# Kernel tuning notes

Measured on AMD Instinct MI355X. Metric: run time of the kernel, lower is better.

## Reference

```python
import jax, jax.numpy as jnp
import numpy as np

N, E, D, ED, H, OUT = 50000, 800000, 128, 32, 16, 128
BN_EPS = 1e-5


def setup_inputs() -> dict:
    key = jax.random.key(0)
    ks = jax.random.split(key, 12)
    s = lambda fan_in: 1.0 / np.sqrt(fan_in)

    x = jax.random.normal(ks[0], (N, D), dtype=jnp.float32)
    edge_idx = jax.random.randint(ks[1], (2, E), 0, N, dtype=jnp.int64)
    edge_feat = jax.random.normal(ks[2], (E, ED), dtype=jnp.float32)

    # edge_mlp: Linear(ED,16) -> GELU -> Linear(16,16); weights stored [in,out]
    eW1 = jax.random.uniform(ks[3], (ED, H), minval=-s(ED), maxval=s(ED), dtype=jnp.float32)
    eb1 = jnp.zeros((H,), jnp.float32)
    eW2 = jax.random.uniform(ks[4], (H, H), minval=-s(H), maxval=s(H), dtype=jnp.float32)
    eb2 = jnp.zeros((H,), jnp.float32)

    # ego_proj: Linear(D, D+16, bias=False)
    ego_W = jax.random.uniform(ks[5], (D, D + H), minval=-s(D), maxval=s(D), dtype=jnp.float32)
    eps = jnp.zeros((1,), jnp.float32)

    # node mlp: Linear(D+16, OUT) -> BN(OUT) -> GELU -> Linear(OUT, OUT)
    W1 = jax.random.uniform(ks[6], (D + H, OUT), minval=-s(D + H), maxval=s(D + H), dtype=jnp.float32)
    b1 = jnp.zeros((OUT,), jnp.float32)
    gamma = jnp.ones((OUT,), jnp.float32)
    beta = jnp.zeros((OUT,), jnp.float32)
    W2 = jax.random.uniform(ks[7], (OUT, OUT), minval=-s(OUT), maxval=s(OUT), dtype=jnp.float32)
    b2 = jnp.zeros((OUT,), jnp.float32)

    return dict(x=x, edge_idx=edge_idx, edge_feat=edge_feat,
                eW1=eW1, eb1=eb1, eW2=eW2, eb2=eb2,
                ego_W=ego_W, eps=eps,
                W1=W1, b1=b1, gamma=gamma, beta=beta, W2=W2, b2=b2)


def reference(x, edge_idx, edge_feat, eW1, eb1, eW2, eb2, ego_W, eps,
              W1, b1, gamma, beta, W2, b2):
    src, dst = edge_idx[0], edge_idx[1]
    # edge MLP (exact GELU, matching torch default)
    e_emb = jax.nn.gelu(edge_feat @ eW1 + eb1, approximate=False) @ eW2 + eb2  # [E,16]
    msg = jnp.concatenate([x[src], e_emb], axis=-1)                            # [E, D+16]
    agg = jax.ops.segment_sum(msg, dst, num_segments=x.shape[0])               # [N, D+16]
    out = (1.0 + eps) * (x @ ego_W) + agg
    # node MLP with BatchNorm1d in training mode (batch stats, biased var)
    h = out @ W1 + b1
    mu = jnp.mean(h, axis=0)
    var = jnp.mean((h - mu) ** 2, axis=0)
    h = (h - mu) * jax.lax.rsqrt(var + BN_EPS) * gamma + beta
    h = jax.nn.gelu(h, approximate=False)
    return h @ W2 + b2
```

## Files before the change

kernel.cpp:

```cpp
#include <hip/hip_runtime.h>
#include <hip/hip_bf16.h>

#define N_NODES 50000
#define E_EDGES 800000
#define D_IN    128
#define ED_IN   32
#define H_HID   16
#define D_CAT   144
#define AGG_LD  144
#define BCAP    48
#define BM      64

typedef __attribute__((ext_vector_type(8))) short bf16x8;
typedef __attribute__((ext_vector_type(4))) float f32x4;

__device__ __forceinline__ float gelu_exact(float v) {
    return 0.5f * v * (1.0f + erff(v * 0.70710678118654752f));
}
__device__ __forceinline__ float4 ld4(const float* p) { return *reinterpret_cast<const float4*>(p); }
__device__ __forceinline__ unsigned short f2bf(float f) {
    unsigned u = __float_as_uint(f);
    return (unsigned short)((u + 0x7FFFu + ((u >> 16) & 1u)) >> 16);
}
__device__ __forceinline__ float bflo(unsigned u) { return __uint_as_float(u << 16); }
__device__ __forceinline__ float bfhi(unsigned u) { return __uint_as_float(u & 0xffff0000u); }
__device__ __forceinline__ unsigned packbf2(float lo, float hi) {
    __hip_bfloat162 h = __float22bfloat162_rn(make_float2(lo, hi));
    return *reinterpret_cast<unsigned*>(&h);
}

__global__ void k_prep(const float* __restrict__ egoW, const float* __restrict__ W1,
                       const float* __restrict__ eps, const float* __restrict__ eW2,
                       const float* __restrict__ eb2, const float* __restrict__ W2,
                       unsigned short* __restrict__ BT, unsigned short* __restrict__ W2T,
                       float* __restrict__ ve, int* __restrict__ cnt,
                       float* __restrict__ stats) {
    const int c = threadIdx.x;
    const int d = blockIdx.x;
    if (d < 128) {
        float acc = 0.f;
        for (int j = 0; j < D_CAT; ++j)
            acc = fmaf(egoW[d * D_CAT + j], W1[j * 128 + c], acc);
        BT[c * 288 + d] = f2bf((1.0f + eps[0]) * acc);
    } else if (d == 128) {
        for (int j = 0; j < 128; ++j)
            BT[c * 288 + 128 + j] = f2bf(W1[j * 128 + c]);
        #pragma unroll
        for (int j = 0; j < H_HID; ++j) {
            float s = 0.f;
            #pragma unroll
            for (int k = 0; k < H_HID; ++k)
                s = fmaf(eW2[j * H_HID + k], W1[(D_IN + k) * 128 + c], s);
            BT[c * 288 + 256 + j] = f2bf(s);
        }
        #pragma unroll
        for (int j = 272; j < 288; ++j) BT[c * 288 + j] = 0;
        float s = 0.f;
        #pragma unroll
        for (int k = 0; k < H_HID; ++k)
            s = fmaf(eb2[k], W1[(D_IN + k) * 128 + c], s);
        ve[c] = s;
    } else if (d == 129) {
        for (int k = 0; k < 128; ++k)
            W2T[c * 128 + k] = f2bf(W2[k * 128 + c]);
    } else if (d < 521) {
        int idx = (d - 130) * 128 + c;
        if (idx < N_NODES) cnt[idx] = 0;
    } else {
        stats[c] = 0.f; stats[128 + c] = 0.f;
    }
}

__global__ __launch_bounds__(256) void k_edge(const float* __restrict__ x,
        uint4* __restrict__ xb, const int* __restrict__ eidx,
        const float* __restrict__ ef, const float* __restrict__ eW1,
        const float* __restrict__ eb1, int* __restrict__ cnt,
        int* __restrict__ bucket, unsigned short* __restrict__ gbuf) {
    const int t = threadIdx.x;
    const int e0 = blockIdx.x * 256;
    const int i = e0 + t;
    const int w = t >> 6, l = t & 63, q = l >> 4, c = l & 15;
    const int eb = e0 + w * 64;

    float4 cx0 = ld4(x + (size_t)i * 8);
    float4 cx1 = ld4(x + (size_t)i * 8 + 4);
    int dst = eidx[E_EDGES + i];
    float4 ef0[4], ef1[4];
    #pragma unroll
    for (int m = 0; m < 4; ++m) {
        const float* ep = ef + (size_t)(eb + m * 16 + c) * ED_IN + q * 8;
        ef0[m] = ld4(ep);
        ef1[m] = ld4(ep + 4);
    }
    float wv[8];
    #pragma unroll
    for (int j = 0; j < 8; ++j) wv[j] = eW1[(q * 8 + j) * 16 + c];
    union { uint4 u; bf16x8 v; } afc;
    afc.u.x = packbf2(wv[0], wv[1]); afc.u.y = packbf2(wv[2], wv[3]);
    afc.u.z = packbf2(wv[4], wv[5]); afc.u.w = packbf2(wv[6], wv[7]);
    const bf16x8 af = afc.v;
    float bias[4];
    #pragma unroll
    for (int j = 0; j < 4; ++j) bias[j] = eb1[q * 4 + j];

    {
        uint4 o;
        o.x = packbf2(cx0.x, cx0.y); o.y = packbf2(cx0.z, cx0.w);
        o.z = packbf2(cx1.x, cx1.y); o.w = packbf2(cx1.z, cx1.w);
        xb[i] = o;
    }
    {
        int pos = atomicAdd(&cnt[dst], 1);
        if (pos < BCAP) bucket[dst * BCAP + pos] = i;
    }
    #pragma unroll
    for (int m = 0; m < 4; ++m) {
        const int em = eb + m * 16 + c;
        union { uint4 u; bf16x8 v; } bc;
        bc.u.x = packbf2(ef0[m].x, ef0[m].y); bc.u.y = packbf2(ef0[m].z, ef0[m].w);
        bc.u.z = packbf2(ef1[m].x, ef1[m].y); bc.u.w = packbf2(ef1[m].z, ef1[m].w);
        f32x4 acc = (f32x4){0.f, 0.f, 0.f, 0.f};
        acc = __builtin_amdgcn_mfma_f32_16x16x32_bf16(af, bc.v, acc, 0, 0, 0);
        uint2 o;
        o.x = packbf2(gelu_exact(acc[0] + bias[0]), gelu_exact(acc[1] + bias[1]));
        o.y = packbf2(gelu_exact(acc[2] + bias[2]), gelu_exact(acc[3] + bias[3]));
        *reinterpret_cast<uint2*>(gbuf + (size_t)em * 16 + q * 4) = o;
    }
}

__global__ __launch_bounds__(256) void k_agg(const unsigned short* __restrict__ xb,
        const int* __restrict__ eidx, const int* __restrict__ cnt,
        const int* __restrict__ bucket, const unsigned short* __restrict__ gbuf,
        unsigned short* __restrict__ aggb) {
    const int wave = threadIdx.x >> 6, lane = threadIdx.x & 63;
    const int q = lane >> 4, ql = lane & 15;
    const int n = blockIdx.x * 4 + wave;
    const int m = min(cnt[n], BCAP);
    int ev = (lane < BCAP) ? bucket[n * BCAP + lane] : 0;
    int sv = (lane < m) ? eidx[ev] : 0;
    float a[8], ae[8];
    #pragma unroll
    for (int i = 0; i < 8; ++i) { a[i] = 0.f; ae[i] = 0.f; }
    const int ng = (m + 3) >> 2;
    #pragma unroll 4
    for (int j = 0; j < ng; ++j) {
        const int eo = 4 * j + q;
        const int s  = __shfl(sv, eo);
        const int ge = __shfl(ev, eo);
        if (eo < m) {
            uint4 v = *reinterpret_cast<const uint4*>(xb + (size_t)s * D_IN + ql * 8);
            a[0] += bflo(v.x); a[1] += bfhi(v.x);
            a[2] += bflo(v.y); a[3] += bfhi(v.y);
            a[4] += bflo(v.z); a[5] += bfhi(v.z);
            a[6] += bflo(v.w); a[7] += bfhi(v.w);
            if (ql < 2) {
                uint4 e = *reinterpret_cast<const uint4*>(gbuf + (size_t)ge * 16 + ql * 8);
                ae[0] += bflo(e.x); ae[1] += bfhi(e.x);
                ae[2] += bflo(e.y); ae[3] += bfhi(e.y);
                ae[4] += bflo(e.z); ae[5] += bfhi(e.z);
                ae[6] += bflo(e.w); ae[7] += bfhi(e.w);
            }
        }
    }
    #pragma unroll
    for (int i = 0; i < 8; ++i) {
        a[i]  += __shfl_xor(a[i], 16);  a[i]  += __shfl_xor(a[i], 32);
        ae[i] += __shfl_xor(ae[i], 16); ae[i] += __shfl_xor(ae[i], 32);
    }
    if (q == 0) {
        unsigned short* ar = aggb + (size_t)n * AGG_LD;
        uint4 o;
        o.x = packbf2(a[0], a[1]); o.y = packbf2(a[2], a[3]);
        o.z = packbf2(a[4], a[5]); o.w = packbf2(a[6], a[7]);
        *reinterpret_cast<uint4*>(ar + ql * 8) = o;
        if (ql < 2) {
            uint4 oe;
            oe.x = packbf2(ae[0], ae[1]); oe.y = packbf2(ae[2], ae[3]);
            oe.z = packbf2(ae[4], ae[5]); oe.w = packbf2(ae[6], ae[7]);
            *reinterpret_cast<uint4*>(ar + D_IN + ql * 8) = oe;
        }
    }
}

__global__ __launch_bounds__(256) void k_gemm1(const unsigned short* __restrict__ xb,
        const unsigned short* __restrict__ aggb, const unsigned short* __restrict__ BT,
        const float* __restrict__ ve, const int* __restrict__ cnt,
        float* __restrict__ h, float* __restrict__ stats) {
    __shared__ short As[64][40];
    __shared__ short Bs[128][40];
    __shared__ float red0[128], red1[128];
    __shared__ float ve_s[128];
    __shared__ int   deg_s[64];
    const int t = threadIdx.x;
    const int row0 = blockIdx.x * BM;
    if (t < 128) { ve_s[t] = ve[t]; red0[t] = 0.f; red1[t] = 0.f; }
    if (t < 64) deg_s[t] = cnt[min(row0 + t, N_NODES - 1)];
    const int w = t >> 6, l = t & 63;
    const int arow = w * 16 + (l & 15);
    const int koff = (l >> 4) * 8;
    f32x4 acc[8];
    #pragma unroll
    for (int ct = 0; ct < 8; ++ct) acc[ct] = (f32x4){0.f, 0.f, 0.f, 0.f};

    #pragma unroll 1
    for (int ch = 0; ch < 9; ++ch) {
        const unsigned short* Ab; int lda, k0, kb;
        if (ch < 4) { Ab = xb;   lda = D_IN;   k0 = ch * 32;       kb = ch * 32; }
        else        { Ab = aggb; lda = AGG_LD; k0 = (ch - 4) * 32; kb = 128 + (ch - 4) * 32; }
        {
            int row = t >> 2, slot = t & 3;
            int r = row0 + row;
            uint4 v = make_uint4(0u, 0u, 0u, 0u);
            if (r < N_NODES) v = *reinterpret_cast<const uint4*>(Ab + (size_t)r * lda + k0 + slot * 8);
            *reinterpret_cast<uint4*>(&As[row][slot * 8]) = v;
        }
        #pragma unroll
        for (int i = 0; i < 2; ++i) {
            int qq = t + 256 * i;
            int row = qq >> 2, slot = qq & 3;
            *reinterpret_cast<uint4*>(&Bs[row][slot * 8]) =
                *reinterpret_cast<const uint4*>(BT + row * 288 + kb + slot * 8);
        }
        __syncthreads();
        bf16x8 af = *reinterpret_cast<const bf16x8*>(&As[arow][koff]);
        #pragma unroll
        for (int ct = 0; ct < 8; ++ct) {
            bf16x8 bfv = *reinterpret_cast<const bf16x8*>(&Bs[ct * 16 + (l & 15)][koff]);
            acc[ct] = __builtin_amdgcn_mfma_f32_16x16x32_bf16(af, bfv, acc[ct], 0, 0, 0);
        }
        __syncthreads();
    }

    #pragma unroll
    for (int ct = 0; ct < 8; ++ct) {
        const int col = ct * 16 + (l & 15);
        float cs0 = 0.f, cs1 = 0.f;
        #pragma unroll
        for (int i = 0; i < 4; ++i) {
            int lr = w * 16 + (l >> 4) * 4 + i;
            int r = row0 + lr;
            float dv = (float)deg_s[lr];
            float v = acc[ct][i] + dv * ve_s[col];
            if (r < N_NODES) { h[(size_t)r * 128 + col] = v; cs0 += v; cs1 += v * v; }
        }
        cs0 += __shfl_xor(cs0, 16); cs0 += __shfl_xor(cs0, 32);
        cs1 += __shfl_xor(cs1, 16); cs1 += __shfl_xor(cs1, 32);
        if (l < 16) { atomicAdd(&red0[col], cs0); atomicAdd(&red1[col], cs1); }
    }
    __syncthreads();
    if (t < 128) {
        unsafeAtomicAdd(stats + t,       red0[t]);
        unsafeAtomicAdd(stats + 128 + t, red1[t]);
    }
}

__global__ __launch_bounds__(256) void k_gemm2(const float* __restrict__ h,
        const float* __restrict__ stats, const float* __restrict__ gamma,
        const float* __restrict__ beta, const unsigned short* __restrict__ W2T,
        const float* __restrict__ b2, float* __restrict__ out) {
    __shared__ short As[64][136];
    __shared__ short Bs[128][40];
    __shared__ float sa[128], sb[128], sc[128];
    const int t = threadIdx.x;
    const int row0 = blockIdx.x * BM;
    if (t < 128) {
        float mu  = stats[t] * (1.0f / N_NODES);
        float var = stats[128 + t] * (1.0f / N_NODES) - mu * mu;
        float av  = gamma[t] * rsqrtf(var + 1e-5f);
        sa[t] = av;
        sb[t] = beta[t] - mu * av;
        sc[t] = b2[t];
    }
    __syncthreads();
    {
        int row = t >> 2, q = t & 3;
        int r = row0 + row;
        #pragma unroll
        for (int i = 0; i < 8; ++i) {
            int c = q * 32 + i * 4;
            float4 v = (r < N_NODES) ? ld4(h + (size_t)r * 128 + c) : make_float4(0.f, 0.f, 0.f, 0.f);
            uint2 pw;
            pw.x = packbf2(gelu_exact(fmaf(sa[c],     v.x, sb[c])),
                           gelu_exact(fmaf(sa[c + 1], v.y, sb[c + 1])));
            pw.y = packbf2(gelu_exact(fmaf(sa[c + 2], v.z, sb[c + 2])),
                           gelu_exact(fmaf(sa[c + 3], v.w, sb[c + 3])));
            *reinterpret_cast<uint2*>(&As[row][c]) = pw;
        }
    }
    const int w = t >> 6, l = t & 63;
    const int arow = w * 16 + (l & 15);
    const int koff = (l >> 4) * 8;
    f32x4 acc[8];
    #pragma unroll
    for (int ct = 0; ct < 8; ++ct) acc[ct] = (f32x4){0.f, 0.f, 0.f, 0.f};

    #pragma unroll 1
    for (int ks = 0; ks < 4; ++ks) {
        #pragma unroll
        for (int i = 0; i < 2; ++i) {
            int qq = t + 256 * i;
            int row = qq >> 2, slot = qq & 3;
            *reinterpret_cast<uint4*>(&Bs[row][slot * 8]) =
                *reinterpret_cast<const uint4*>(W2T + row * 128 + ks * 32 + slot * 8);
        }
        __syncthreads();
        bf16x8 af = *reinterpret_cast<const bf16x8*>(&As[arow][ks * 32 + koff]);
        #pragma unroll
        for (int ct = 0; ct < 8; ++ct) {
            bf16x8 bfv = *reinterpret_cast<const bf16x8*>(&Bs[ct * 16 + (l & 15)][koff]);
            acc[ct] = __builtin_amdgcn_mfma_f32_16x16x32_bf16(af, bfv, acc[ct], 0, 0, 0);
        }
        __syncthreads();
    }
    #pragma unroll
    for (int ct = 0; ct < 8; ++ct) {
        const int col = ct * 16 + (l & 15);
        #pragma unroll
        for (int i = 0; i < 4; ++i) {
            int r = row0 + w * 16 + (l >> 4) * 4 + i;
            if (r < N_NODES) out[(size_t)r * 128 + col] = acc[ct][i] + sc[col];
        }
    }
}

extern "C" void kernel_launch(void* const* d_in, const int* in_sizes, int n_in,
                              void* d_out, int out_size, void* d_ws, size_t ws_size,
                              hipStream_t stream) {
    const float* x     = (const float*)d_in[0];
    const int*   eidx  = (const int*)d_in[1];
    const float* ef    = (const float*)d_in[2];
    const float* eW1   = (const float*)d_in[3];
    const float* eb1   = (const float*)d_in[4];
    const float* eW2   = (const float*)d_in[5];
    const float* eb2   = (const float*)d_in[6];
    const float* egoW  = (const float*)d_in[7];
    const float* eps   = (const float*)d_in[8];
    const float* W1    = (const float*)d_in[9];
    const float* gamma = (const float*)d_in[11];
    const float* beta  = (const float*)d_in[12];
    const float* W2    = (const float*)d_in[13];
    const float* b2    = (const float*)d_in[14];
    float* out = (float*)d_out;

    char* ws = (char*)d_ws;
    unsigned short* aggb = (unsigned short*)ws;
    unsigned short* xb   = (unsigned short*)(ws + 14400128);
    float* stats  = (float*)(ws + 27200128);
    unsigned short* BT  = (unsigned short*)(ws + 27201152);
    unsigned short* W2T = (unsigned short*)(ws + 27274880);
    float* ve     = (float*)(ws + 27307648);
    int*   cnt    = (int*)(ws + 27308160);
    int*   bucket = (int*)(ws + 27508864);
    unsigned short* gbuf = (unsigned short*)d_out;
    float* h      = out;

    k_prep<<<dim3(522), dim3(128), 0, stream>>>(egoW, W1, eps, eW2, eb2, W2, BT, W2T, ve,
                                                cnt, stats);
    k_edge<<<dim3(E_EDGES / 256), dim3(256), 0, stream>>>(x, (uint4*)xb, eidx, ef, eW1, eb1,
                                                          cnt, bucket, gbuf);
    k_agg<<<dim3(N_NODES / 4), dim3(256), 0, stream>>>(xb, eidx, cnt, bucket, gbuf, aggb);
    k_gemm1<<<dim3((N_NODES + BM - 1) / BM), dim3(256), 0, stream>>>(xb, aggb, BT, ve,
                                                                     cnt, h, stats);
    k_gemm2<<<dim3((N_NODES + BM - 1) / BM), dim3(256), 0, stream>>>(h, stats, gamma, beta,
                                                                     W2T, b2, out);
}
```

Before: 172.5 us.

## Drop bf16 copy of x; gather fp32 x directly and fold weight prep into edge kernel

The bf16 staging copy of x is no longer written in the edge kernel. The aggregation kernel now gathers fp32 rows of x directly, and the first GEMM converts x to bf16 while loading it into shared memory. Weight preprocessing moves into extra blocks of the edge kernel, and counter/stats zeroing moves into a small separate kernel. This removes a 12.8 MB write and its later reread, but doubles the bytes read by the random gather in aggregation.

```diff
diff --git a/kernel.cpp b/kernel.cpp
--- a/kernel.cpp
+++ b/kernel.cpp
@@ -10,6 +10,7 @@
 #define AGG_LD  144
 #define BCAP    48
 #define BM      64
+#define EDGE_BLKS (E_EDGES / 256)
 
 typedef __attribute__((ext_vector_type(8))) short bf16x8;
 typedef __attribute__((ext_vector_type(4))) float f32x4;
@@ -29,61 +30,61 @@
     return *reinterpret_cast<unsigned*>(&h);
 }
 
-__global__ void k_prep(const float* __restrict__ egoW, const float* __restrict__ W1,
-                       const float* __restrict__ eps, const float* __restrict__ eW2,
-                       const float* __restrict__ eb2, const float* __restrict__ W2,
-                       unsigned short* __restrict__ BT, unsigned short* __restrict__ W2T,
-                       float* __restrict__ ve, int* __restrict__ cnt,
-                       float* __restrict__ stats) {
-    const int c = threadIdx.x;
-    const int d = blockIdx.x;
-    if (d < 128) {
-        float acc = 0.f;
-        for (int j = 0; j < D_CAT; ++j)
-            acc = fmaf(egoW[d * D_CAT + j], W1[j * 128 + c], acc);
-        BT[c * 288 + d] = f2bf((1.0f + eps[0]) * acc);
-    } else if (d == 128) {
-        for (int j = 0; j < 128; ++j)
-            BT[c * 288 + 128 + j] = f2bf(W1[j * 128 + c]);
-        #pragma unroll
-        for (int j = 0; j < H_HID; ++j) {
+__global__ __launch_bounds__(256) void k_zero(int* __restrict__ cnt, float* __restrict__ stats) {
+    int i = blockIdx.x * 256 + threadIdx.x;
+    if (i < 12500) *reinterpret_cast<int4*>(cnt + i * 4) = make_int4(0, 0, 0, 0);
+    if (blockIdx.x == 49 && threadIdx.x < 64)
+        *reinterpret_cast<float4*>(stats + threadIdx.x * 4) = make_float4(0.f, 0.f, 0.f, 0.f);
+}
+
+__global__ __launch_bounds__(256) void k_edge(const float* __restrict__ x,
+        const int* __restrict__ eidx, const float* __restrict__ ef,
+        const float* __restrict__ eW1, const float* __restrict__ eb1,
+        const float* __restrict__ egoW, const float* __restrict__ W1,
+        const float* __restrict__ eps, const float* __restrict__ eW2,
+        const float* __restrict__ eb2, const float* __restrict__ W2,
+        int* __restrict__ cnt, int* __restrict__ bucket,
+        unsigned short* __restrict__ gbuf, unsigned short* __restrict__ BT,
+        unsigned short* __restrict__ W2T, float* __restrict__ ve) {
+    const int b = blockIdx.x, t = threadIdx.x;
+    if (b >= EDGE_BLKS) {
+        if (t >= 128) return;
+        const int c = t;
+        const int d = b - EDGE_BLKS;
+        if (d < 128) {
+            float acc = 0.f;
+            for (int j = 0; j < D_CAT; ++j)
+                acc = fmaf(egoW[d * D_CAT + j], W1[j * 128 + c], acc);
+            BT[c * 288 + d] = f2bf((1.0f + eps[0]) * acc);
+        } else if (d == 128) {
+            for (int j = 0; j < 128; ++j)
+                BT[c * 288 + 128 + j] = f2bf(W1[j * 128 + c]);
+            #pragma unroll
+            for (int j = 0; j < H_HID; ++j) {
+                float s = 0.f;
+                #pragma unroll
+                for (int k = 0; k < H_HID; ++k)
+                    s = fmaf(eW2[j * H_HID + k], W1[(D_IN + k) * 128 + c], s);
+                BT[c * 288 + 256 + j] = f2bf(s);
+            }
+            #pragma unroll
+            for (int j = 272; j < 288; ++j) BT[c * 288 + j] = 0;
             float s = 0.f;
             #pragma unroll
             for (int k = 0; k < H_HID; ++k)
-                s = fmaf(eW2[j * H_HID + k], W1[(D_IN + k) * 128 + c], s);
-            BT[c * 288 + 256 + j] = f2bf(s);
-        }
-        #pragma unroll
-        for (int j = 272; j < 288; ++j) BT[c * 288 + j] = 0;
-        float s = 0.f;
-        #pragma unroll
-        for (int k = 0; k < H_HID; ++k)
-            s = fmaf(eb2[k], W1[(D_IN + k) * 128 + c], s);
-        ve[c] = s;
-    } else if (d == 129) {
-        for (int k = 0; k < 128; ++k)
-            W2T[c * 128 + k] = f2bf(W2[k * 128 + c]);
-    } else if (d < 521) {
-        int idx = (d - 130) * 128 + c;
-        if (idx < N_NODES) cnt[idx] = 0;
-    } else {
-        stats[c] = 0.f; stats[128 + c] = 0.f;
-    }
-}
-
-__global__ __launch_bounds__(256) void k_edge(const float* __restrict__ x,
-        uint4* __restrict__ xb, const int* __restrict__ eidx,
-        const float* __restrict__ ef, const float* __restrict__ eW1,
-        const float* __restrict__ eb1, int* __restrict__ cnt,
-        int* __restrict__ bucket, unsigned short* __restrict__ gbuf) {
-    const int t = threadIdx.x;
-    const int e0 = blockIdx.x * 256;
+                s = fmaf(eb2[k], W1[(D_IN + k) * 128 + c], s);
+            ve[c] = s;
+        } else {
+            for (int k = 0; k < 128; ++k)
+                W2T[c * 128 + k] = f2bf(W2[k * 128 + c]);
+        }
+        return;
+    }
+    const int e0 = b * 256;
     const int i = e0 + t;
     const int w = t >> 6, l = t & 63, q = l >> 4, c = l & 15;
     const int eb = e0 + w * 64;
 
-    float4 cx0 = ld4(x + (size_t)i * 8);
-    float4 cx1 = ld4(x + (size_t)i * 8 + 4);
     int dst = eidx[E_EDGES + i];
     float4 ef0[4], ef1[4];
     #pragma unroll
@@ -103,12 +104,6 @@
     #pragma unroll
     for (int j = 0; j < 4; ++j) bias[j] = eb1[q * 4 + j];
 
-    {
-        uint4 o;
-        o.x = packbf2(cx0.x, cx0.y); o.y = packbf2(cx0.z, cx0.w);
-        o.z = packbf2(cx1.x, cx1.y); o.w = packbf2(cx1.z, cx1.w);
-        xb[i] = o;
-    }
     {
         int pos = atomicAdd(&cnt[dst], 1);
         if (pos < BCAP) bucket[dst * BCAP + pos] = i;
@@ -128,7 +123,7 @@
     }
 }
 
-__global__ __launch_bounds__(256) void k_agg(const unsigned short* __restrict__ xb,
+__global__ __launch_bounds__(256) void k_agg(const float* __restrict__ x,
         const int* __restrict__ eidx, const int* __restrict__ cnt,
         const int* __restrict__ bucket, const unsigned short* __restrict__ gbuf,
         unsigned short* __restrict__ aggb) {
@@ -148,11 +143,10 @@
         const int s  = __shfl(sv, eo);
         const int ge = __shfl(ev, eo);
         if (eo < m) {
-            uint4 v = *reinterpret_cast<const uint4*>(xb + (size_t)s * D_IN + ql * 8);
-            a[0] += bflo(v.x); a[1] += bfhi(v.x);
-            a[2] += bflo(v.y); a[3] += bfhi(v.y);
-            a[4] += bflo(v.z); a[5] += bfhi(v.z);
-            a[6] += bflo(v.w); a[7] += bfhi(v.w);
+            const float* xp = x + (size_t)s * D_IN + ql * 8;
+            float4 v0 = ld4(xp), v1 = ld4(xp + 4);
+            a[0] += v0.x; a[1] += v0.y; a[2] += v0.z; a[3] += v0.w;
+            a[4] += v1.x; a[5] += v1.y; a[6] += v1.z; a[7] += v1.w;
             if (ql < 2) {
                 uint4 e = *reinterpret_cast<const uint4*>(gbuf + (size_t)ge * 16 + ql * 8);
                 ae[0] += bflo(e.x); ae[1] += bfhi(e.x);
@@ -182,7 +176,7 @@
     }
 }
 
-__global__ __launch_bounds__(256) void k_gemm1(const unsigned short* __restrict__ xb,
+__global__ __launch_bounds__(256) void k_gemm1(const float* __restrict__ x,
         const unsigned short* __restrict__ aggb, const unsigned short* __restrict__ BT,
         const float* __restrict__ ve, const int* __restrict__ cnt,
         float* __restrict__ h, float* __restrict__ stats) {
@@ -204,22 +198,32 @@
 
     #pragma unroll 1
     for (int ch = 0; ch < 9; ++ch) {
-        const unsigned short* Ab; int lda, k0, kb;
-        if (ch < 4) { Ab = xb;   lda = D_IN;   k0 = ch * 32;       kb = ch * 32; }
-        else        { Ab = aggb; lda = AGG_LD; k0 = (ch - 4) * 32; kb = 128 + (ch - 4) * 32; }
-        {
-            int row = t >> 2, slot = t & 3;
-            int r = row0 + row;
+        const int row = t >> 2, slot = t & 3;
+        const int r = row0 + row;
+        if (ch < 4) {
+            const int k0 = ch * 32;
+            uint4 sv = make_uint4(0u, 0u, 0u, 0u);
+            if (r < N_NODES) {
+                const float* xp = x + (size_t)r * D_IN + k0 + slot * 8;
+                float4 v0 = ld4(xp), v1 = ld4(xp + 4);
+                sv.x = packbf2(v0.x, v0.y); sv.y = packbf2(v0.z, v0.w);
+                sv.z = packbf2(v1.x, v1.y); sv.w = packbf2(v1.z, v1.w);
+            }
+            *reinterpret_cast<uint4*>(&As[row][slot * 8]) = sv;
+        } else {
+            const int k0 = (ch - 4) * 32;
             uint4 v = make_uint4(0u, 0u, 0u, 0u);
-            if (r < N_NODES) v = *reinterpret_cast<const uint4*>(Ab + (size_t)r * lda + k0 + slot * 8);
+            if (r < N_NODES)
+                v = *reinterpret_cast<const uint4*>(aggb + (size_t)r * AGG_LD + k0 + slot * 8);
             *reinterpret_cast<uint4*>(&As[row][slot * 8]) = v;
         }
+        const int kb = (ch < 4) ? ch * 32 : 128 + (ch - 4) * 32;
         #pragma unroll
         for (int i = 0; i < 2; ++i) {
             int qq = t + 256 * i;
-            int row = qq >> 2, slot = qq & 3;
-            *reinterpret_cast<uint4*>(&Bs[row][slot * 8]) =
-                *reinterpret_cast<const uint4*>(BT + row * 288 + kb + slot * 8);
+            int brow = qq >> 2, bslot = qq & 3;
+            *reinterpret_cast<uint4*>(&Bs[brow][bslot * 8]) =
+                *reinterpret_cast<const uint4*>(BT + brow * 288 + kb + bslot * 8);
         }
         __syncthreads();
         bf16x8 af = *reinterpret_cast<const bf16x8*>(&As[arow][koff]);
@@ -344,22 +348,21 @@
 
     char* ws = (char*)d_ws;
     unsigned short* aggb = (unsigned short*)ws;
-    unsigned short* xb   = (unsigned short*)(ws + 14400128);
-    float* stats  = (float*)(ws + 27200128);
-    unsigned short* BT  = (unsigned short*)(ws + 27201152);
-    unsigned short* W2T = (unsigned short*)(ws + 27274880);
-    float* ve     = (float*)(ws + 27307648);
-    int*   cnt    = (int*)(ws + 27308160);
-    int*   bucket = (int*)(ws + 27508864);
+    float* stats  = (float*)(ws + 14400128);
+    unsigned short* BT  = (unsigned short*)(ws + 14401152);
+    unsigned short* W2T = (unsigned short*)(ws + 14474880);
+    float* ve     = (float*)(ws + 14507648);
+    int*   cnt    = (int*)(ws + 14508160);
+    int*   bucket = (int*)(ws + 14708864);
     unsigned short* gbuf = (unsigned short*)d_out;
     float* h      = out;
 
-    k_prep<<<dim3(522), dim3(128), 0, stream>>>(egoW, W1, eps, eW2, eb2, W2, BT, W2T, ve,
-                                                cnt, stats);
-    k_edge<<<dim3(E_EDGES / 256), dim3(256), 0, stream>>>(x, (uint4*)xb, eidx, ef, eW1, eb1,
-                                                          cnt, bucket, gbuf);
-    k_agg<<<dim3(N_NODES / 4), dim3(256), 0, stream>>>(xb, eidx, cnt, bucket, gbuf, aggb);
-    k_gemm1<<<dim3((N_NODES + BM - 1) / BM), dim3(256), 0, stream>>>(xb, aggb, BT, ve,
+    k_zero<<<dim3(50), dim3(256), 0, stream>>>(cnt, stats);
+    k_edge<<<dim3(EDGE_BLKS + 130), dim3(256), 0, stream>>>(x, eidx, ef, eW1, eb1,
+                                                            egoW, W1, eps, eW2, eb2, W2,
+                                                            cnt, bucket, gbuf, BT, W2T, ve);
+    k_agg<<<dim3(N_NODES / 4), dim3(256), 0, stream>>>(x, eidx, cnt, bucket, gbuf, aggb);
+    k_gemm1<<<dim3((N_NODES + BM - 1) / BM), dim3(256), 0, stream>>>(x, aggb, BT, ve,
                                                                      cnt, h, stats);
     k_gemm2<<<dim3((N_NODES + BM - 1) / BM), dim3(256), 0, stream>>>(h, stats, gamma, beta,
                                                                      W2T, b2, out);
```

New measurement: 195.3 us. 1.13x slower.
